# Kernel tuning notes

Hardware: AMD Instinct MI355X
Metric: run time of the kernel (lower is better)

Reference implementation:

```python
import jax, jax.numpy as jnp
import numpy as np

B, N, D = 16, 2048, 1024   # batch, num_windows, input_dim
H, A = 256, 128            # feature head dim, attention hidden dim
EPS = 1e-5                 # torch LayerNorm eps
NEG = -1e9                 # finite mask value (avoids NaN in softmax/grads)
KMAX = max(1, N // 10)     # static upper bound on per-sample top-k


def setup_inputs() -> dict:
    key = jax.random.key(0)
    ks = jax.random.split(key, 6)
    rn = lambda k, shape, sc: jax.random.normal(k, shape, jnp.float32) * sc
    return {
        "x": rn(ks[0], (B, N, D), 1.0),
        "lengths": jax.random.randint(ks[1], (B,), 0, N, dtype=jnp.int64)
                   if jax.config.jax_enable_x64 else
                   jax.random.randint(ks[1], (B,), 0, N, dtype=jnp.int32),
        # feature_head: Linear(D,H) + LayerNorm(H) (+ GELU, dropout=eval no-op)
        "W1": rn(ks[2], (H, D), D ** -0.5), "b1": jnp.zeros((H,), jnp.float32),
        "ln_g": jnp.ones((H,), jnp.float32), "ln_b": jnp.zeros((H,), jnp.float32),
        # attention: Linear(H,A) -> tanh -> Linear(A,1)
        "Wa1": rn(ks[3], (A, H), H ** -0.5), "ba1": jnp.zeros((A,), jnp.float32),
        "Wa2": rn(ks[4], (1, A), A ** -0.5), "ba2": jnp.zeros((1,), jnp.float32),
        # classifier: Linear(H,1)
        "Wc": rn(ks[5], (1, H), H ** -0.5), "bc": jnp.zeros((1,), jnp.float32),
    }


def reference(x, lengths, W1, b1, ln_g, ln_b, Wa1, ba1, Wa2, ba2, Wc, bc):
    # feature head: Linear + LayerNorm + exact GELU (dropout is identity in eval)
    h = jnp.einsum('bnd,hd->bnh', x, W1) + b1
    mu = h.mean(-1, keepdims=True)
    var = h.var(-1, keepdims=True)  # biased, as in torch LayerNorm
    h = (h - mu) * jax.lax.rsqrt(var + EPS) * ln_g + ln_b
    h = jax.nn.gelu(h, approximate=False)

    instance_scores = jnp.einsum('bnh,oh->bno', h, Wc)[..., 0] + bc[0]   # (B, N)
    a_hidden = jnp.tanh(jnp.einsum('bnh,ah->bna', h, Wa1) + ba1)
    attn_logits = jnp.einsum('bna,oa->bno', a_hidden, Wa2)[..., 0] + ba2[0]  # (B, N)

    T = lengths                                    # (B,)
    mask = jnp.arange(N)[None, :] < T[:, None]     # (B, N) valid-window mask

    # masked softmax attention pooling over the first T windows
    w = jax.nn.softmax(jnp.where(mask, attn_logits, NEG), axis=1)
    attn_score = jnp.sum(w * instance_scores * mask, axis=1)

    # dynamic top-k: k = max(1, floor(0.1*T)); take static KMAX then mask ranks
    k_i = jnp.maximum(1, T // 10)                  # (B,)
    vals, _ = jax.lax.top_k(jnp.where(mask, instance_scores, NEG), KMAX)
    rank_mask = jnp.arange(KMAX)[None, :] < k_i[:, None]
    topk_mean = jnp.sum(vals * rank_mask, axis=1) / k_i.astype(vals.dtype)

    video = jnp.where(T > 0, 0.5 * attn_score + 0.5 * topk_mean,
                      jnp.zeros((), vals.dtype))
    return video[:, None], instance_scores
```

## Files before the change

### kernel.cpp

```cpp
#include <hip/hip_runtime.h>
#include <hip/hip_bf16.h>
#include <cmath>

#define Bn 16
#define Nn 2048
#define Dn 1024
#define Hn 256
#define An 128

typedef __bf16 bf16x8 __attribute__((ext_vector_type(8)));
typedef float f32x4 __attribute__((ext_vector_type(4)));
typedef unsigned short ushort8v __attribute__((ext_vector_type(8)));

static __device__ __forceinline__ unsigned short f2bf(float f) {
  unsigned u = __float_as_uint(f);
  u += 0x7fffu + ((u >> 16) & 1u);
  return (unsigned short)(u >> 16);
}

static __device__ __forceinline__ bf16x8 cvt8(const float4 a, const float4 b) {
  bf16x8 r;
  r[0] = (__bf16)a.x; r[1] = (__bf16)a.y; r[2] = (__bf16)a.z; r[3] = (__bf16)a.w;
  r[4] = (__bf16)b.x; r[5] = (__bf16)b.y; r[6] = (__bf16)b.z; r[7] = (__bf16)b.w;
  return r;
}

static __device__ __forceinline__ void glds16(const void* g, void* l) {
  __builtin_amdgcn_global_load_lds(
      (const __attribute__((address_space(1))) unsigned int*)g,
      (__attribute__((address_space(3))) unsigned int*)l, 16, 0, 0);
}

__global__ __launch_bounds__(256) void conv_bf16_kernel(
    const float* __restrict__ W1, const float* __restrict__ Wa1,
    unsigned short* __restrict__ w1o, unsigned short* __restrict__ wa1o) {
  const int bid = blockIdx.x;
  const float* in;
  unsigned short* out;
  int i;
  if (bid < 128) { in = W1;  out = w1o;  i = (bid * 256 + threadIdx.x) << 3; }
  else           { in = Wa1; out = wa1o; i = ((bid - 128) * 256 + threadIdx.x) << 3; }
  const float4 a = *(const float4*)(in + i);
  const float4 b = *(const float4*)(in + i + 4);
  ushort8v u;
  u[0] = f2bf(a.x); u[1] = f2bf(a.y); u[2] = f2bf(a.z); u[3] = f2bf(a.w);
  u[4] = f2bf(b.x); u[5] = f2bf(b.y); u[6] = f2bf(b.z); u[7] = f2bf(b.w);
  *(ushort8v*)(out + i) = u;
}

__global__ __launch_bounds__(256) void fused_main(
    const float* __restrict__ x,
    const float* __restrict__ b1,
    const float* __restrict__ ln_g,
    const float* __restrict__ ln_b,
    const float* __restrict__ ba1,
    const float* __restrict__ Wa2,
    const float* __restrict__ ba2,
    const float* __restrict__ Wc,
    const float* __restrict__ bc,
    const unsigned short* __restrict__ W1bf,
    const unsigned short* __restrict__ Wa1bf,
    float* __restrict__ scores_out,
    float* __restrict__ logits_out)
{
  __shared__ __align__(16) __bf16 AB[4096 + 16384];
  __shared__ float red[64][8];

  const int tid  = threadIdx.x;
  const int wv   = tid >> 6;
  const int lane = tid & 63;
  const int l15  = lane & 15;
  const int lhi  = lane >> 4;
  const int rg   = wv >> 1;
  const int cw   = wv & 1;

  const int gr0 = blockIdx.x << 6;
  const int bb  = blockIdx.x >> 5;
  const int n0  = (blockIdx.x & 31) << 6;

  char* ABb = (char*)AB;

  f32x4 acc[2][8];
  #pragma unroll
  for (int rf = 0; rf < 2; ++rf)
    #pragma unroll
    for (int cf = 0; cf < 8; ++cf)
      acc[rf][cf] = (f32x4){0.f, 0.f, 0.f, 0.f};

  const int st_row   = tid >> 2;
  const int st_lslot = (tid & 3) ^ ((tid >> 3) & 3);
  const float* xbase = x + (size_t)(gr0 + st_row) * Dn + (st_lslot << 3);

  auto issueB = [&](int p, int kc) {
    const int kk = kc << 5;
    char* Bb = ABb + 8192 + p * 16384;
    #pragma unroll
    for (int i = 0; i < 4; ++i) {
      const int c = (wv << 8) + (i << 6) + lane;
      const int h = c >> 2;
      const int lslot = (c & 3) ^ ((c >> 3) & 3);
      glds16(W1bf + (size_t)h * Dn + kk + (lslot << 3),
             ABb + 8192 + p * 16384 + ((wv << 8) + (i << 6)) * 16);
      (void)Bb;
    }
  };

  auto computeStep = [&](int p) {
    const char* Ab = ABb + p * 4096;
    const char* Bb = ABb + 8192 + p * 16384;
    bf16x8 afrag[2];
    #pragma unroll
    for (int rf = 0; rf < 2; ++rf) {
      const int row = (rg << 5) + (rf << 4) + l15;
      afrag[rf] = *(const bf16x8*)(Ab + row * 64 + ((lhi ^ ((row >> 1) & 3)) << 4));
    }
    #pragma unroll
    for (int cf = 0; cf < 8; ++cf) {
      const int h = (cw << 7) + (cf << 4) + l15;
      const bf16x8 bfr = *(const bf16x8*)(Bb + h * 64 + ((lhi ^ ((h >> 1) & 3)) << 4));
      acc[0][cf] = __builtin_amdgcn_mfma_f32_16x16x32_bf16(afrag[0], bfr, acc[0][cf], 0, 0, 0);
      acc[1][cf] = __builtin_amdgcn_mfma_f32_16x16x32_bf16(afrag[1], bfr, acc[1][cf], 0, 0, 0);
    }
  };

  {
    issueB(0, 0);
    const float4 a0 = *(const float4*)(xbase);
    const float4 a1 = *(const float4*)(xbase + 4);
    *(bf16x8*)(ABb + (tid << 4)) = cvt8(a0, a1);
  }
  __syncthreads();

  int p = 0;
  for (int kc = 0; kc < 32; ++kc) {
    const int np = p ^ 1;
    float4 na0, na1;
    if (kc < 31) {
      issueB(np, kc + 1);
      const float* xs = xbase + ((kc + 1) << 5);
      na0 = *(const float4*)(xs);
      na1 = *(const float4*)(xs + 4);
    }
    computeStep(p);
    if (kc < 31)
      *(bf16x8*)(ABb + np * 4096 + (tid << 4)) = cvt8(na0, na1);
    __syncthreads();
    p = np;
  }

  const float bc0 = bc[0];
  float b1v[8];
  #pragma unroll
  for (int cf = 0; cf < 8; ++cf) b1v[cf] = b1[(cw << 7) + (cf << 4) + l15];

  float ps[2][4], ps2[2][4];
  #pragma unroll
  for (int rf = 0; rf < 2; ++rf)
    #pragma unroll
    for (int r = 0; r < 4; ++r) { ps[rf][r] = 0.f; ps2[rf][r] = 0.f; }

  #pragma unroll
  for (int rf = 0; rf < 2; ++rf)
    #pragma unroll
    for (int cf = 0; cf < 8; ++cf)
      #pragma unroll
      for (int r = 0; r < 4; ++r) {
        const float v = acc[rf][cf][r] + b1v[cf];
        acc[rf][cf][r] = v;
        ps[rf][r] += v; ps2[rf][r] += v * v;
      }
  #pragma unroll
  for (int rf = 0; rf < 2; ++rf)
    #pragma unroll
    for (int r = 0; r < 4; ++r)
      #pragma unroll
      for (int s = 1; s < 16; s <<= 1) {
        ps[rf][r]  += __shfl_xor(ps[rf][r],  s, 64);
        ps2[rf][r] += __shfl_xor(ps2[rf][r], s, 64);
      }
  if (l15 == 0) {
    #pragma unroll
    for (int rf = 0; rf < 2; ++rf)
      #pragma unroll
      for (int r = 0; r < 4; ++r) {
        const int rowb = (rg << 5) + (rf << 4) + (lhi << 2) + r;
        red[rowb][cw << 1]       = ps[rf][r];
        red[rowb][(cw << 1) + 1] = ps2[rf][r];
      }
  }
  __syncthreads();

  float mu[2][4], inv[2][4];
  #pragma unroll
  for (int rf = 0; rf < 2; ++rf)
    #pragma unroll
    for (int r = 0; r < 4; ++r) {
      const int rowb = (rg << 5) + (rf << 4) + (lhi << 2) + r;
      const float s = red[rowb][0] + red[rowb][2];
      const float q = red[rowb][1] + red[rowb][3];
      const float m = s * (1.f / 256.f);
      const float var = q * (1.f / 256.f) - m * m;
      mu[rf][r] = m;
      inv[rf][r] = rsqrtf(var + 1e-5f);
    }

  float gv[8], bv[8], wcv[8];
  #pragma unroll
  for (int cf = 0; cf < 8; ++cf) {
    const int col = (cw << 7) + (cf << 4) + l15;
    gv[cf] = ln_g[col]; bv[cf] = ln_b[col]; wcv[cf] = Wc[col];
  }
  float sc[2][4];
  #pragma unroll
  for (int rf = 0; rf < 2; ++rf)
    #pragma unroll
    for (int r = 0; r < 4; ++r) sc[rf][r] = 0.f;

  #pragma unroll
  for (int rf = 0; rf < 2; ++rf)
    #pragma unroll
    for (int cf = 0; cf < 8; ++cf)
      #pragma unroll
      for (int r = 0; r < 4; ++r) {
        float v = (acc[rf][cf][r] - mu[rf][r]) * inv[rf][r] * gv[cf] + bv[cf];
        v = 0.5f * v * (1.f + erff(v * 0.70710678118654752f));
        sc[rf][r] += v * wcv[cf];
        const int rowb = (rg << 5) + (rf << 4) + (lhi << 2) + r;
        const int col  = (cw << 7) + (cf << 4) + l15;
        *(__bf16*)(ABb + rowb * 512 + (((col >> 3) ^ (rowb & 7)) << 4) + ((col & 7) << 1)) = (__bf16)v;
      }
  #pragma unroll
  for (int rf = 0; rf < 2; ++rf)
    #pragma unroll
    for (int r = 0; r < 4; ++r)
      #pragma unroll
      for (int s = 1; s < 16; s <<= 1)
        sc[rf][r] += __shfl_xor(sc[rf][r], s, 64);
  if (l15 == 0) {
    #pragma unroll
    for (int rf = 0; rf < 2; ++rf)
      #pragma unroll
      for (int r = 0; r < 4; ++r) {
        const int rowb = (rg << 5) + (rf << 4) + (lhi << 2) + r;
        red[rowb][4 + cw] = sc[rf][r];
      }
  }
  __syncthreads();
  if (tid < 64)
    scores_out[(size_t)bb * Nn + n0 + tid] = red[tid][4] + red[tid][5] + bc0;

  f32x4 acc2[8];
  #pragma unroll
  for (int cf = 0; cf < 8; ++cf) acc2[cf] = (f32x4){0.f, 0.f, 0.f, 0.f};

  const int r16 = (wv << 4) + l15;
  #pragma unroll
  for (int ks = 0; ks < 8; ++ks) {
    const bf16x8 af = *(const bf16x8*)(ABb + r16 * 512 + ((((ks << 2) + lhi) ^ (r16 & 7)) << 4));
    #pragma unroll
    for (int cf = 0; cf < 8; ++cf) {
      const bf16x8 bfr = *(const bf16x8*)((const __bf16*)Wa1bf +
                          (size_t)((cf << 4) + l15) * Hn + (ks << 5) + (lhi << 3));
      acc2[cf] = __builtin_amdgcn_mfma_f32_16x16x32_bf16(af, bfr, acc2[cf], 0, 0, 0);
    }
  }
  const float ba20 = ba2[0];
  float lg[4] = {0.f, 0.f, 0.f, 0.f};
  #pragma unroll
  for (int cf = 0; cf < 8; ++cf) {
    const int col = (cf << 4) + l15;
    const float bav = ba1[col], w2v = Wa2[col];
    #pragma unroll
    for (int r = 0; r < 4; ++r) {
      const float t = acc2[cf][r] + bav;
      const float e = __expf(2.f * t);
      const float th = 1.f - 2.f / (e + 1.f);
      lg[r] += th * w2v;
    }
  }
  #pragma unroll
  for (int r = 0; r < 4; ++r)
    #pragma unroll
    for (int s = 1; s < 16; s <<= 1) lg[r] += __shfl_xor(lg[r], s, 64);
  if (l15 == 0) {
    #pragma unroll
    for (int r = 0; r < 4; ++r)
      logits_out[(size_t)bb * Nn + n0 + (wv << 4) + (lhi << 2) + r] = lg[r] + ba20;
  }
}

__global__ __launch_bounds__(256) void finalize_kernel(
    const int* __restrict__ lengths,
    const float* __restrict__ scores,
    const float* __restrict__ logits,
    float* __restrict__ video)
{
  const int b = blockIdx.x;
  const int tid = threadIdx.x;
  __shared__ float sS[Nn];
  __shared__ float sL[Nn];
  __shared__ unsigned skey[Nn];
  __shared__ float sred[8];

  const int T = lengths[b];
  for (int i = tid; i < Nn; i += 256) {
    sS[i] = scores[(size_t)b * Nn + i];
    sL[i] = logits[(size_t)b * Nn + i];
  }
  __syncthreads();
  if (T <= 0) { if (tid == 0) video[b] = 0.f; return; }

  float m = -3.0e38f;
  for (int i = tid; i < T; i += 256) m = fmaxf(m, sL[i]);
  #pragma unroll
  for (int s = 1; s < 64; s <<= 1) m = fmaxf(m, __shfl_xor(m, s, 64));
  if ((tid & 63) == 0) sred[tid >> 6] = m;
  __syncthreads();
  m = fmaxf(fmaxf(sred[0], sred[1]), fmaxf(sred[2], sred[3]));
  __syncthreads();

  float se = 0.f, swe = 0.f;
  for (int i = tid; i < T; i += 256) {
    const float e = expf(sL[i] - m);
    se += e; swe += e * sS[i];
  }
  #pragma unroll
  for (int s = 1; s < 64; s <<= 1) { se += __shfl_xor(se, s, 64); swe += __shfl_xor(swe, s, 64); }
  if ((tid & 63) == 0) { sred[tid >> 6] = se; sred[4 + (tid >> 6)] = swe; }
  __syncthreads();
  se  = sred[0] + sred[1] + sred[2] + sred[3];
  swe = sred[4] + sred[5] + sred[6] + sred[7];
  __syncthreads();
  const float attn = swe / se;

  for (int i = tid; i < T; i += 256) {
    const unsigned u = __float_as_uint(sS[i]);
    skey[i] = (u & 0x80000000u) ? ~u : (u | 0x80000000u);
  }
  __syncthreads();
  const int k = max(1, T / 10);
  unsigned ans = 0u;
  for (int bit = 31; bit >= 0; --bit) {
    const unsigned cand = ans | (1u << bit);
    int c = 0;
    for (int i = tid; i < T; i += 256) c += (skey[i] >= cand) ? 1 : 0;
    #pragma unroll
    for (int s = 1; s < 64; s <<= 1) c += __shfl_xor(c, s, 64);
    if ((tid & 63) == 0) sred[tid >> 6] = (float)c;
    __syncthreads();
    c = (int)(sred[0] + sred[1] + sred[2] + sred[3]);
    __syncthreads();
    if (c >= k) ans = cand;
  }
  int cgt = 0; float sgt = 0.f;
  for (int i = tid; i < T; i += 256) {
    if (skey[i] > ans) { cgt++; sgt += sS[i]; }
  }
  #pragma unroll
  for (int s = 1; s < 64; s <<= 1) { cgt += __shfl_xor(cgt, s, 64); sgt += __shfl_xor(sgt, s, 64); }
  if ((tid & 63) == 0) { sred[tid >> 6] = (float)cgt; sred[4 + (tid >> 6)] = sgt; }
  __syncthreads();
  cgt = (int)(sred[0] + sred[1] + sred[2] + sred[3]);
  sgt = sred[4] + sred[5] + sred[6] + sred[7];

  const unsigned ub = (ans & 0x80000000u) ? (ans ^ 0x80000000u) : ~ans;
  const float kth = __uint_as_float(ub);
  const float topk = (sgt + (float)(k - cgt) * kth) / (float)k;
  if (tid == 0) video[b] = 0.5f * attn + 0.5f * topk;
}

extern "C" void kernel_launch(void* const* d_in, const int* in_sizes, int n_in,
                              void* d_out, int out_size, void* d_ws, size_t ws_size,
                              hipStream_t stream) {
  const float* x    = (const float*)d_in[0];
  const int*   len  = (const int*)  d_in[1];
  const float* W1   = (const float*)d_in[2];
  const float* b1   = (const float*)d_in[3];
  const float* ln_g = (const float*)d_in[4];
  const float* ln_b = (const float*)d_in[5];
  const float* Wa1  = (const float*)d_in[6];
  const float* ba1  = (const float*)d_in[7];
  const float* Wa2  = (const float*)d_in[8];
  const float* ba2  = (const float*)d_in[9];
  const float* Wc   = (const float*)d_in[10];
  const float* bc   = (const float*)d_in[11];

  float* out    = (float*)d_out;
  float* video  = out;
  float* scores = out + Bn;

  char* ws = (char*)d_ws;
  float*          logits = (float*)ws;
  unsigned short* wa1bf  = (unsigned short*)(ws + (size_t)Bn * Nn * 4);
  unsigned short* w1bf   = (unsigned short*)(ws + (size_t)Bn * Nn * 4 + (size_t)An * Hn * 2);

  hipLaunchKernelGGL(conv_bf16_kernel, dim3(144), dim3(256), 0, stream, W1, Wa1, w1bf, wa1bf);
  hipLaunchKernelGGL(fused_main, dim3(Bn * Nn / 64), dim3(256), 0, stream,
                     x, b1, ln_g, ln_b, ba1, Wa2, ba2, Wc, bc,
                     w1bf, wa1bf, scores, logits);
  hipLaunchKernelGGL(finalize_kernel, dim3(Bn), dim3(256), 0, stream, len, scores, logits, video);
}
```

Baseline: 95.69 us.

## Double K-tile to 64, prefetch x two stages ahead with explicit waitcnt barriers

The GEMM main loop now uses a 64-wide K chunk (16 iterations instead of 32), with a new 8-way XOR swizzle for the A and B LDS tiles. x rows are register-prefetched two chunks ahead and the barriers are replaced by explicit s_waitcnt vmcnt/lgkmcnt plus s_barrier, with sched_barriers to pin the issue order. The aim is to halve barrier count and hide global-load latency better. In exchange LDS use grows to 80KB, which limits occupancy, and register pressure rises from the extra prefetch buffers.

```diff
diff --git a/kernel.cpp b/kernel.cpp
--- a/kernel.cpp
+++ b/kernel.cpp
@@ -11,6 +11,17 @@
 typedef __bf16 bf16x8 __attribute__((ext_vector_type(8)));
 typedef float f32x4 __attribute__((ext_vector_type(4)));
 typedef unsigned short ushort8v __attribute__((ext_vector_type(8)));
+
+#define LDSA(p) ((p) * 8192)
+#define LDSB(p) (16384 + (p) * 32768)
+#define LDSH    49152
+#define LDSRED  8192
+
+#define PIPE_BARRIER(N) do {                                        \
+    asm volatile("s_waitcnt vmcnt(" #N ") lgkmcnt(0)" ::: "memory"); \
+    __builtin_amdgcn_s_barrier();                                   \
+    __builtin_amdgcn_sched_barrier(0);                              \
+  } while (0)
 
 static __device__ __forceinline__ unsigned short f2bf(float f) {
   unsigned u = __float_as_uint(f);
@@ -63,8 +74,7 @@
     float* __restrict__ scores_out,
     float* __restrict__ logits_out)
 {
-  __shared__ __align__(16) __bf16 AB[4096 + 16384];
-  __shared__ float red[64][8];
+  __shared__ __align__(16) char lds[81920];
 
   const int tid  = threadIdx.x;
   const int wv   = tid >> 6;
@@ -78,8 +88,6 @@
   const int bb  = blockIdx.x >> 5;
   const int n0  = (blockIdx.x & 31) << 6;
 
-  char* ABb = (char*)AB;
-
   f32x4 acc[2][8];
   #pragma unroll
   for (int rf = 0; rf < 2; ++rf)
@@ -87,66 +95,76 @@
     for (int cf = 0; cf < 8; ++cf)
       acc[rf][cf] = (f32x4){0.f, 0.f, 0.f, 0.f};
 
-  const int st_row   = tid >> 2;
-  const int st_lslot = (tid & 3) ^ ((tid >> 3) & 3);
-  const float* xbase = x + (size_t)(gr0 + st_row) * Dn + (st_lslot << 3);
+  const int arow = tid >> 2;
+  const int aq   = tid & 3;
+  const float* xbase = x + (size_t)(gr0 + arow) * Dn + (aq << 4);
+  char* awr0 = lds + arow * 128 + (((aq << 1)       ^ (arow & 7)) << 4);
+  char* awr1 = lds + arow * 128 + ((((aq << 1) | 1) ^ (arow & 7)) << 4);
+
+  const unsigned short* bsrc = W1bf + (size_t)(wv * 64 + (lane >> 3)) * Dn
+                               + (((lane & 7) ^ ((lane >> 3) & 7)) << 3);
+
+  const int axor = l15 & 7;
 
   auto issueB = [&](int p, int kc) {
-    const int kk = kc << 5;
-    char* Bb = ABb + 8192 + p * 16384;
-    #pragma unroll
-    for (int i = 0; i < 4; ++i) {
-      const int c = (wv << 8) + (i << 6) + lane;
-      const int h = c >> 2;
-      const int lslot = (c & 3) ^ ((c >> 3) & 3);
-      glds16(W1bf + (size_t)h * Dn + kk + (lslot << 3),
-             ABb + 8192 + p * 16384 + ((wv << 8) + (i << 6)) * 16);
-      (void)Bb;
+    #pragma unroll
+    for (int i = 0; i < 8; ++i)
+      glds16(bsrc + (size_t)i * 8 * Dn + (kc << 6),
+             lds + LDSB(p) + (wv * 64 + i * 8) * 128);
+  };
+  auto loadX = [&](float4* v, int kc) {
+    #pragma unroll
+    for (int j = 0; j < 4; ++j)
+      v[j] = *(const float4*)(xbase + (kc << 6) + (j << 2));
+  };
+  auto writeA = [&](int p, const float4* v) {
+    *(bf16x8*)(awr0 + LDSA(p)) = cvt8(v[0], v[1]);
+    *(bf16x8*)(awr1 + LDSA(p)) = cvt8(v[2], v[3]);
+  };
+  auto computeStep = [&](int p) {
+    const char* Ab = lds + LDSA(p);
+    const char* Bb = lds + LDSB(p);
+    #pragma unroll
+    for (int ks = 0; ks < 2; ++ks) {
+      const int so = (((ks << 2) + lhi) ^ axor) << 4;
+      const bf16x8 aA = *(const bf16x8*)(Ab + ((rg << 5) + l15) * 128 + so);
+      const bf16x8 aB = *(const bf16x8*)(Ab + ((rg << 5) + 16 + l15) * 128 + so);
+      #pragma unroll
+      for (int cf = 0; cf < 8; ++cf) {
+        const bf16x8 bfr = *(const bf16x8*)(Bb + ((cw << 7) + (cf << 4) + l15) * 128 + so);
+        acc[0][cf] = __builtin_amdgcn_mfma_f32_16x16x32_bf16(aA, bfr, acc[0][cf], 0, 0, 0);
+        acc[1][cf] = __builtin_amdgcn_mfma_f32_16x16x32_bf16(aB, bfr, acc[1][cf], 0, 0, 0);
+      }
     }
   };
 
-  auto computeStep = [&](int p) {
-    const char* Ab = ABb + p * 4096;
-    const char* Bb = ABb + 8192 + p * 16384;
-    bf16x8 afrag[2];
-    #pragma unroll
-    for (int rf = 0; rf < 2; ++rf) {
-      const int row = (rg << 5) + (rf << 4) + l15;
-      afrag[rf] = *(const bf16x8*)(Ab + row * 64 + ((lhi ^ ((row >> 1) & 3)) << 4));
+  float4 xr0[4], xr1[4];
+  issueB(0, 0);
+  __builtin_amdgcn_sched_barrier(0);
+  loadX(xr0, 0);
+  loadX(xr1, 1);
+  __builtin_amdgcn_sched_barrier(0);
+  writeA(0, xr0);
+  PIPE_BARRIER(4);
+
+  #pragma unroll
+  for (int kc = 0; kc < 16; ++kc) {
+    const int p = kc & 1;
+    const int np = p ^ 1;
+    if (kc < 15) issueB(np, kc + 1);
+    __builtin_amdgcn_sched_barrier(0);
+    if (kc < 14) loadX((kc & 1) ? xr1 : xr0, kc + 2);
+    __builtin_amdgcn_sched_barrier(0);
+    computeStep(p);
+    if (kc < 15) {
+      writeA(np, np ? xr1 : xr0);
+      if (kc < 14) PIPE_BARRIER(4);
+      else         PIPE_BARRIER(0);
     }
-    #pragma unroll
-    for (int cf = 0; cf < 8; ++cf) {
-      const int h = (cw << 7) + (cf << 4) + l15;
-      const bf16x8 bfr = *(const bf16x8*)(Bb + h * 64 + ((lhi ^ ((h >> 1) & 3)) << 4));
-      acc[0][cf] = __builtin_amdgcn_mfma_f32_16x16x32_bf16(afrag[0], bfr, acc[0][cf], 0, 0, 0);
-      acc[1][cf] = __builtin_amdgcn_mfma_f32_16x16x32_bf16(afrag[1], bfr, acc[1][cf], 0, 0, 0);
-    }
-  };
-
-  {
-    issueB(0, 0);
-    const float4 a0 = *(const float4*)(xbase);
-    const float4 a1 = *(const float4*)(xbase + 4);
-    *(bf16x8*)(ABb + (tid << 4)) = cvt8(a0, a1);
-  }
-  __syncthreads();
-
-  int p = 0;
-  for (int kc = 0; kc < 32; ++kc) {
-    const int np = p ^ 1;
-    float4 na0, na1;
-    if (kc < 31) {
-      issueB(np, kc + 1);
-      const float* xs = xbase + ((kc + 1) << 5);
-      na0 = *(const float4*)(xs);
-      na1 = *(const float4*)(xs + 4);
-    }
-    computeStep(p);
-    if (kc < 31)
-      *(bf16x8*)(ABb + np * 4096 + (tid << 4)) = cvt8(na0, na1);
-    __syncthreads();
-    p = np;
-  }
+  }
+  __syncthreads();
+
+  float (*red)[8] = (float(*)[8])(lds + LDSRED);
 
   const float bc0 = bc[0];
   float b1v[8];
@@ -227,7 +245,8 @@
         sc[rf][r] += v * wcv[cf];
         const int rowb = (rg << 5) + (rf << 4) + (lhi << 2) + r;
         const int col  = (cw << 7) + (cf << 4) + l15;
-        *(__bf16*)(ABb + rowb * 512 + (((col >> 3) ^ (rowb & 7)) << 4) + ((col & 7) << 1)) = (__bf16)v;
+        *(__bf16*)(lds + LDSH + rowb * 512 + (((col >> 3) ^ (rowb & 7)) << 4)
+                   + ((col & 7) << 1)) = (__bf16)v;
       }
   #pragma unroll
   for (int rf = 0; rf < 2; ++rf)
@@ -256,7 +275,8 @@
   const int r16 = (wv << 4) + l15;
   #pragma unroll
   for (int ks = 0; ks < 8; ++ks) {
-    const bf16x8 af = *(const bf16x8*)(ABb + r16 * 512 + ((((ks << 2) + lhi) ^ (r16 & 7)) << 4));
+    const bf16x8 af = *(const bf16x8*)(lds + LDSH + r16 * 512 +
+                        ((((ks << 2) + lhi) ^ (r16 & 7)) << 4));
     #pragma unroll
     for (int cf = 0; cf < 8; ++cf) {
       const bf16x8 bfr = *(const bf16x8*)((const __bf16*)Wa1bf +
```

Result: faster. 88.90 us (-7.1%).

## Restructure GEMM mainloop: register-direct W1 loads, 256-wide x chunks in LDS

Applied to the files above, without the earlier changes.

Rewrites the main GEMM pipeline. W1 bf16 fragments are now loaded straight from global memory into registers, double-buffered one k-step ahead, instead of being staged through LDS with global_load_lds. x is loaded in 256-column chunks into 16 float4 registers and written to a double-buffered 64 KB LDS region, so a barrier is needed only every 8 k-steps rather than every step. The aim is fewer barriers and less LDS traffic, at the cost of higher register pressure and LDS use, which may lower occupancy, plus redundant global W1 loads per wave.

```diff
diff --git a/kernel.cpp b/kernel.cpp
--- a/kernel.cpp
+++ b/kernel.cpp
@@ -12,6 +12,12 @@
 typedef float f32x4 __attribute__((ext_vector_type(4)));
 typedef unsigned short ushort8v __attribute__((ext_vector_type(8)));
 
+#define LDS_BARRIER do {                                   \
+    asm volatile("s_waitcnt lgkmcnt(0)" ::: "memory");     \
+    __builtin_amdgcn_s_barrier();                          \
+    __builtin_amdgcn_sched_barrier(0);                     \
+  } while (0)
+
 static __device__ __forceinline__ unsigned short f2bf(float f) {
   unsigned u = __float_as_uint(f);
   u += 0x7fffu + ((u >> 16) & 1u);
@@ -23,12 +29,6 @@
   r[0] = (__bf16)a.x; r[1] = (__bf16)a.y; r[2] = (__bf16)a.z; r[3] = (__bf16)a.w;
   r[4] = (__bf16)b.x; r[5] = (__bf16)b.y; r[6] = (__bf16)b.z; r[7] = (__bf16)b.w;
   return r;
-}
-
-static __device__ __forceinline__ void glds16(const void* g, void* l) {
-  __builtin_amdgcn_global_load_lds(
-      (const __attribute__((address_space(1))) unsigned int*)g,
-      (__attribute__((address_space(3))) unsigned int*)l, 16, 0, 0);
 }
 
 __global__ __launch_bounds__(256) void conv_bf16_kernel(
@@ -63,8 +63,7 @@
     float* __restrict__ scores_out,
     float* __restrict__ logits_out)
 {
-  __shared__ __align__(16) __bf16 AB[4096 + 16384];
-  __shared__ float red[64][8];
+  __shared__ __align__(16) char lds[65536 + 2048];
 
   const int tid  = threadIdx.x;
   const int wv   = tid >> 6;
@@ -78,8 +77,6 @@
   const int bb  = blockIdx.x >> 5;
   const int n0  = (blockIdx.x & 31) << 6;
 
-  char* ABb = (char*)AB;
-
   f32x4 acc[2][8];
   #pragma unroll
   for (int rf = 0; rf < 2; ++rf)
@@ -87,66 +84,64 @@
     for (int cf = 0; cf < 8; ++cf)
       acc[rf][cf] = (f32x4){0.f, 0.f, 0.f, 0.f};
 
-  const int st_row   = tid >> 2;
-  const int st_lslot = (tid & 3) ^ ((tid >> 3) & 3);
-  const float* xbase = x + (size_t)(gr0 + st_row) * Dn + (st_lslot << 3);
-
-  auto issueB = [&](int p, int kc) {
-    const int kk = kc << 5;
-    char* Bb = ABb + 8192 + p * 16384;
-    #pragma unroll
-    for (int i = 0; i < 4; ++i) {
-      const int c = (wv << 8) + (i << 6) + lane;
-      const int h = c >> 2;
-      const int lslot = (c & 3) ^ ((c >> 3) & 3);
-      glds16(W1bf + (size_t)h * Dn + kk + (lslot << 3),
-             ABb + 8192 + p * 16384 + ((wv << 8) + (i << 6)) * 16);
-      (void)Bb;
+  const int sr = tid >> 2, sq = tid & 3;
+  const float* xbase = x + (size_t)(gr0 + sr) * Dn + (sq << 6);
+  char* awbase = lds + sr * 512;
+
+  const int arow0 = (rg << 5) + l15;
+  const int arow1 = arow0 + 16;
+  const int ax    = l15 & 7;
+
+  const __bf16* wbL = (const __bf16*)W1bf + (size_t)((cw << 7) + l15) * Dn + (lhi << 3);
+
+  float4 xr[16];
+  bf16x8 Ba[8], Bb[8];
+
+  #define LOADX(ph) do {                                                     \
+      _Pragma("unroll") for (int j = 0; j < 16; ++j)                         \
+        xr[j] = *(const float4*)(xbase + ((ph) << 8) + (j << 2));            \
+    } while (0)
+  #define WRITEA(pbuf) do {                                                  \
+      char* ab_ = awbase + (pbuf) * 32768;                                   \
+      _Pragma("unroll") for (int j = 0; j < 8; ++j) {                        \
+        const bf16x8 v_ = cvt8(xr[2 * j], xr[2 * j + 1]);                    \
+        *(bf16x8*)(ab_ + ((((sq << 3) + j) ^ (sr & 7)) << 4)) = v_;          \
+      }                                                                      \
+    } while (0)
+  #define ISSUEB(arr, Kk) do {                                               \
+      const __bf16* bp_ = wbL + ((Kk) << 5);                                 \
+      _Pragma("unroll") for (int cf = 0; cf < 8; ++cf)                       \
+        arr[cf] = *(const bf16x8*)(bp_ + (size_t)(cf << 4) * Dn);            \
+    } while (0)
+  #define DOMFMA(arr, Kk) do {                                               \
+      const char* ab_ = lds + (((Kk) >> 3) & 1) * 32768;                     \
+      const int sl_ = ((Kk) & 7) << 2;                                       \
+      const bf16x8 a0_ = *(const bf16x8*)(ab_ + arow0 * 512 + (((sl_ + lhi) ^ ax) << 4)); \
+      const bf16x8 a1_ = *(const bf16x8*)(ab_ + arow1 * 512 + (((sl_ + lhi) ^ ax) << 4)); \
+      _Pragma("unroll") for (int cf = 0; cf < 8; ++cf) {                     \
+        acc[0][cf] = __builtin_amdgcn_mfma_f32_16x16x32_bf16(a0_, arr[cf], acc[0][cf], 0, 0, 0); \
+        acc[1][cf] = __builtin_amdgcn_mfma_f32_16x16x32_bf16(a1_, arr[cf], acc[1][cf], 0, 0, 0); \
+      }                                                                      \
+    } while (0)
+
+  LOADX(0);
+  ISSUEB(Ba, 0);
+  WRITEA(0);
+  LDS_BARRIER;
+
+  #pragma unroll
+  for (int K = 0; K < 32; ++K) {
+    if (K < 31) { if (K & 1) ISSUEB(Ba, K + 1); else ISSUEB(Bb, K + 1); }
+    if ((K & 7) == 0 && K < 24) LOADX((K >> 3) + 1);
+    if (K & 1) DOMFMA(Bb, K); else DOMFMA(Ba, K);
+    if ((K & 7) == 7 && K < 31) {
+      WRITEA(((K >> 3) + 1) & 1);
+      LDS_BARRIER;
     }
-  };
-
-  auto computeStep = [&](int p) {
-    const char* Ab = ABb + p * 4096;
-    const char* Bb = ABb + 8192 + p * 16384;
-    bf16x8 afrag[2];
-    #pragma unroll
-    for (int rf = 0; rf < 2; ++rf) {
-      const int row = (rg << 5) + (rf << 4) + l15;
-      afrag[rf] = *(const bf16x8*)(Ab + row * 64 + ((lhi ^ ((row >> 1) & 3)) << 4));
-    }
-    #pragma unroll
-    for (int cf = 0; cf < 8; ++cf) {
-      const int h = (cw << 7) + (cf << 4) + l15;
-      const bf16x8 bfr = *(const bf16x8*)(Bb + h * 64 + ((lhi ^ ((h >> 1) & 3)) << 4));
-      acc[0][cf] = __builtin_amdgcn_mfma_f32_16x16x32_bf16(afrag[0], bfr, acc[0][cf], 0, 0, 0);
-      acc[1][cf] = __builtin_amdgcn_mfma_f32_16x16x32_bf16(afrag[1], bfr, acc[1][cf], 0, 0, 0);
-    }
-  };
-
-  {
-    issueB(0, 0);
-    const float4 a0 = *(const float4*)(xbase);
-    const float4 a1 = *(const float4*)(xbase + 4);
-    *(bf16x8*)(ABb + (tid << 4)) = cvt8(a0, a1);
-  }
-  __syncthreads();
-
-  int p = 0;
-  for (int kc = 0; kc < 32; ++kc) {
-    const int np = p ^ 1;
-    float4 na0, na1;
-    if (kc < 31) {
-      issueB(np, kc + 1);
-      const float* xs = xbase + ((kc + 1) << 5);
-      na0 = *(const float4*)(xs);
-      na1 = *(const float4*)(xs + 4);
-    }
-    computeStep(p);
-    if (kc < 31)
-      *(bf16x8*)(ABb + np * 4096 + (tid << 4)) = cvt8(na0, na1);
-    __syncthreads();
-    p = np;
-  }
+  }
+  __syncthreads();
+
+  float (*red)[8] = (float(*)[8])(lds + 65536);
 
   const float bc0 = bc[0];
   float b1v[8];
@@ -227,7 +222,8 @@
         sc[rf][r] += v * wcv[cf];
         const int rowb = (rg << 5) + (rf << 4) + (lhi << 2) + r;
         const int col  = (cw << 7) + (cf << 4) + l15;
-        *(__bf16*)(ABb + rowb * 512 + (((col >> 3) ^ (rowb & 7)) << 4) + ((col & 7) << 1)) = (__bf16)v;
+        *(__bf16*)(lds + rowb * 512 + (((col >> 3) ^ (rowb & 7)) << 4)
+                   + ((col & 7) << 1)) = (__bf16)v;
       }
   #pragma unroll
   for (int rf = 0; rf < 2; ++rf)
@@ -256,7 +252,8 @@
   const int r16 = (wv << 4) + l15;
   #pragma unroll
   for (int ks = 0; ks < 8; ++ks) {
-    const bf16x8 af = *(const bf16x8*)(ABb + r16 * 512 + ((((ks << 2) + lhi) ^ (r16 & 7)) << 4));
+    const bf16x8 af = *(const bf16x8*)(lds + r16 * 512 +
+                        ((((ks << 2) + lhi) ^ (r16 & 7)) << 4));
     #pragma unroll
     for (int cf = 0; cf < 8; ++cf) {
       const bf16x8 bfr = *(const bf16x8*)((const __bf16*)Wa1bf +
```

Result: slower. 137.5 us (+43.7%).

## Split attention GEMM into separate kernel and prepack swizzled weights for register-staged loads

Applied to the files above, without the earlier changes.

Weights are prepacked on device into the exact swizzled LDS tile order, so the main GEMM loads B with plain coalesced vector loads staged through registers instead of global_load_lds. The loop is fully unrolled with s_setprio, uses a lighter lgkmcnt barrier, and raises occupancy to three blocks per CU. The attention-hidden GEMM moves into a second kernel that reads a bf16 h buffer from global memory and keeps Wa1 in LDS. This trades an extra 16 MB write and read of h and one more launch for a lighter main kernel.

```diff
diff --git a/kernel.cpp b/kernel.cpp
--- a/kernel.cpp
+++ b/kernel.cpp
@@ -11,6 +11,13 @@
 typedef __bf16 bf16x8 __attribute__((ext_vector_type(8)));
 typedef float f32x4 __attribute__((ext_vector_type(4)));
 typedef unsigned short ushort8v __attribute__((ext_vector_type(8)));
+typedef unsigned int uint4v __attribute__((ext_vector_type(4)));
+
+#define LDS_BARRIER do {                                   \
+    asm volatile("s_waitcnt lgkmcnt(0)" ::: "memory");     \
+    __builtin_amdgcn_s_barrier();                          \
+    __builtin_amdgcn_sched_barrier(0);                     \
+  } while (0)
 
 static __device__ __forceinline__ unsigned short f2bf(float f) {
   unsigned u = __float_as_uint(f);
@@ -25,46 +32,50 @@
   return r;
 }
 
-static __device__ __forceinline__ void glds16(const void* g, void* l) {
-  __builtin_amdgcn_global_load_lds(
-      (const __attribute__((address_space(1))) unsigned int*)g,
-      (__attribute__((address_space(3))) unsigned int*)l, 16, 0, 0);
-}
-
-__global__ __launch_bounds__(256) void conv_bf16_kernel(
+__global__ __launch_bounds__(256) void pack_weights(
     const float* __restrict__ W1, const float* __restrict__ Wa1,
-    unsigned short* __restrict__ w1o, unsigned short* __restrict__ wa1o) {
-  const int bid = blockIdx.x;
-  const float* in;
-  unsigned short* out;
-  int i;
-  if (bid < 128) { in = W1;  out = w1o;  i = (bid * 256 + threadIdx.x) << 3; }
-  else           { in = Wa1; out = wa1o; i = ((bid - 128) * 256 + threadIdx.x) << 3; }
-  const float4 a = *(const float4*)(in + i);
-  const float4 b = *(const float4*)(in + i + 4);
-  ushort8v u;
-  u[0] = f2bf(a.x); u[1] = f2bf(a.y); u[2] = f2bf(a.z); u[3] = f2bf(a.w);
-  u[4] = f2bf(b.x); u[5] = f2bf(b.y); u[6] = f2bf(b.z); u[7] = f2bf(b.w);
-  *(ushort8v*)(out + i) = u;
-}
-
-__global__ __launch_bounds__(256) void fused_main(
+    unsigned short* __restrict__ w1p, unsigned short* __restrict__ wa1p) {
+  const int idx = blockIdx.x * 256 + threadIdx.x;
+  const float* src;
+  unsigned short* dst;
+  if (blockIdx.x < 128) {
+    const int kc  = idx >> 10;
+    const int u   = idx & 1023;
+    const int col = u >> 2;
+    const int lq  = (u & 3) ^ ((col >> 1) & 3);
+    src = W1 + (size_t)col * Dn + (kc << 5) + (lq << 3);
+    dst = w1p + (size_t)idx * 8;
+  } else {
+    const int v   = idx - 32768;
+    const int row = v >> 5;
+    const int ls  = (v & 31) ^ (row & 7);
+    src = Wa1 + (size_t)row * Hn + (ls << 3);
+    dst = wa1p + (size_t)v * 8;
+  }
+  const float4 a = *(const float4*)src;
+  const float4 b = *(const float4*)(src + 4);
+  ushort8v o;
+  o[0] = f2bf(a.x); o[1] = f2bf(a.y); o[2] = f2bf(a.z); o[3] = f2bf(a.w);
+  o[4] = f2bf(b.x); o[5] = f2bf(b.y); o[6] = f2bf(b.z); o[7] = f2bf(b.w);
+  *(ushort8v*)dst = o;
+}
+
+#define K1A(p) ((p) * 4096)
+#define K1B(p) (8192 + (p) * 16384)
+#define K1H    8192
+#define K1RED  40960
+__global__ __launch_bounds__(256, 3) void gemm_ln_kernel(
     const float* __restrict__ x,
     const float* __restrict__ b1,
     const float* __restrict__ ln_g,
     const float* __restrict__ ln_b,
-    const float* __restrict__ ba1,
-    const float* __restrict__ Wa2,
-    const float* __restrict__ ba2,
     const float* __restrict__ Wc,
     const float* __restrict__ bc,
-    const unsigned short* __restrict__ W1bf,
-    const unsigned short* __restrict__ Wa1bf,
+    const unsigned short* __restrict__ w1p,
     float* __restrict__ scores_out,
-    float* __restrict__ logits_out)
+    unsigned short* __restrict__ h_out)
 {
-  __shared__ __align__(16) __bf16 AB[4096 + 16384];
-  __shared__ float red[64][8];
+  __shared__ __align__(16) char lds[43008];
 
   const int tid  = threadIdx.x;
   const int wv   = tid >> 6;
@@ -75,10 +86,8 @@
   const int cw   = wv & 1;
 
   const int gr0 = blockIdx.x << 6;
-  const int bb  = blockIdx.x >> 5;
-  const int n0  = (blockIdx.x & 31) << 6;
-
-  char* ABb = (char*)AB;
+  const int bb  = gr0 >> 11;
+  const int n0  = gr0 & (Nn - 1);
 
   f32x4 acc[2][8];
   #pragma unroll
@@ -87,66 +96,66 @@
     for (int cf = 0; cf < 8; ++cf)
       acc[rf][cf] = (f32x4){0.f, 0.f, 0.f, 0.f};
 
-  const int st_row   = tid >> 2;
-  const int st_lslot = (tid & 3) ^ ((tid >> 3) & 3);
-  const float* xbase = x + (size_t)(gr0 + st_row) * Dn + (st_lslot << 3);
-
-  auto issueB = [&](int p, int kc) {
-    const int kk = kc << 5;
-    char* Bb = ABb + 8192 + p * 16384;
-    #pragma unroll
-    for (int i = 0; i < 4; ++i) {
-      const int c = (wv << 8) + (i << 6) + lane;
-      const int h = c >> 2;
-      const int lslot = (c & 3) ^ ((c >> 3) & 3);
-      glds16(W1bf + (size_t)h * Dn + kk + (lslot << 3),
-             ABb + 8192 + p * 16384 + ((wv << 8) + (i << 6)) * 16);
-      (void)Bb;
+  const int arow = tid >> 2, aq = tid & 3;
+  const int aphys = aq ^ ((arow >> 1) & 3);
+  const float* xsrc = x + (size_t)(gr0 + arow) * Dn + (aq << 3);
+  const int awoff = arow * 64 + (aphys << 4);
+
+  const unsigned short* bsrc = w1p + (size_t)tid * 8;
+
+  const int bx    = lhi ^ ((l15 >> 1) & 3);
+  const int aoff  = ((rg << 5) + l15) * 64 + (bx << 4);
+  const int boff  = (((cw << 7) + l15) * 64) + (bx << 4);
+
+  float4 xs0, xs1;
+  uint4v Bst[4];
+
+  auto loadStage = [&](int kc) {
+    xs0 = *(const float4*)(xsrc + (kc << 5));
+    xs1 = *(const float4*)(xsrc + (kc << 5) + 4);
+    const unsigned short* bp = bsrc + (size_t)kc * 8192;
+    #pragma unroll
+    for (int q = 0; q < 4; ++q)
+      Bst[q] = *(const uint4v*)(bp + q * 2048);
+  };
+  auto writeStage = [&](int p) {
+    *(bf16x8*)(lds + K1A(p) + awoff) = cvt8(xs0, xs1);
+    #pragma unroll
+    for (int q = 0; q < 4; ++q)
+      *(uint4v*)(lds + K1B(p) + ((q << 8) + tid) * 16) = Bst[q];
+  };
+  auto computeStep = [&](int p) {
+    const char* Ab = lds + K1A(p);
+    const char* Bb = lds + K1B(p);
+    __builtin_amdgcn_s_setprio(1);
+    const bf16x8 aA = *(const bf16x8*)(Ab + aoff);
+    const bf16x8 aB = *(const bf16x8*)(Ab + aoff + 1024);
+    #pragma unroll
+    for (int cf = 0; cf < 8; ++cf) {
+      const bf16x8 bfr = *(const bf16x8*)(Bb + boff + cf * 1024);
+      acc[0][cf] = __builtin_amdgcn_mfma_f32_16x16x32_bf16(aA, bfr, acc[0][cf], 0, 0, 0);
+      acc[1][cf] = __builtin_amdgcn_mfma_f32_16x16x32_bf16(aB, bfr, acc[1][cf], 0, 0, 0);
     }
+    __builtin_amdgcn_s_setprio(0);
   };
 
-  auto computeStep = [&](int p) {
-    const char* Ab = ABb + p * 4096;
-    const char* Bb = ABb + 8192 + p * 16384;
-    bf16x8 afrag[2];
-    #pragma unroll
-    for (int rf = 0; rf < 2; ++rf) {
-      const int row = (rg << 5) + (rf << 4) + l15;
-      afrag[rf] = *(const bf16x8*)(Ab + row * 64 + ((lhi ^ ((row >> 1) & 3)) << 4));
+  loadStage(0);
+  writeStage(0);
+  LDS_BARRIER;
+
+  #pragma unroll
+  for (int kc = 0; kc < 32; ++kc) {
+    const int p = kc & 1;
+    if (kc < 31) loadStage(kc + 1);
+    computeStep(p);
+    if (kc < 31) {
+      writeStage(p ^ 1);
+      LDS_BARRIER;
     }
-    #pragma unroll
-    for (int cf = 0; cf < 8; ++cf) {
-      const int h = (cw << 7) + (cf << 4) + l15;
-      const bf16x8 bfr = *(const bf16x8*)(Bb + h * 64 + ((lhi ^ ((h >> 1) & 3)) << 4));
-      acc[0][cf] = __builtin_amdgcn_mfma_f32_16x16x32_bf16(afrag[0], bfr, acc[0][cf], 0, 0, 0);
-      acc[1][cf] = __builtin_amdgcn_mfma_f32_16x16x32_bf16(afrag[1], bfr, acc[1][cf], 0, 0, 0);
-    }
-  };
-
-  {
-    issueB(0, 0);
-    const float4 a0 = *(const float4*)(xbase);
-    const float4 a1 = *(const float4*)(xbase + 4);
-    *(bf16x8*)(ABb + (tid << 4)) = cvt8(a0, a1);
-  }
-  __syncthreads();
-
-  int p = 0;
-  for (int kc = 0; kc < 32; ++kc) {
-    const int np = p ^ 1;
-    float4 na0, na1;
-    if (kc < 31) {
-      issueB(np, kc + 1);
-      const float* xs = xbase + ((kc + 1) << 5);
-      na0 = *(const float4*)(xs);
-      na1 = *(const float4*)(xs + 4);
-    }
-    computeStep(p);
-    if (kc < 31)
-      *(bf16x8*)(ABb + np * 4096 + (tid << 4)) = cvt8(na0, na1);
-    __syncthreads();
-    p = np;
-  }
+  }
+  __syncthreads();
+
+  float (*red)[8] = (float(*)[8])(lds + K1RED);
 
   const float bc0 = bc[0];
   float b1v[8];
@@ -227,7 +236,8 @@
         sc[rf][r] += v * wcv[cf];
         const int rowb = (rg << 5) + (rf << 4) + (lhi << 2) + r;
         const int col  = (cw << 7) + (cf << 4) + l15;
-        *(__bf16*)(ABb + rowb * 512 + (((col >> 3) ^ (rowb & 7)) << 4) + ((col & 7) << 1)) = (__bf16)v;
+        *(__bf16*)(lds + K1H + rowb * 512 + (((col >> 3) ^ (rowb & 7)) << 4)
+                   + ((col & 7) << 1)) = (__bf16)v;
       }
   #pragma unroll
   for (int rf = 0; rf < 2; ++rf)
@@ -249,18 +259,61 @@
   if (tid < 64)
     scores_out[(size_t)bb * Nn + n0 + tid] = red[tid][4] + red[tid][5] + bc0;
 
+  #pragma unroll
+  for (int j = 0; j < 8; ++j) {
+    const int g   = (j << 8) + tid;
+    const int row = g >> 5;
+    const int c   = g & 31;
+    const bf16x8 hv = *(const bf16x8*)(lds + K1H + row * 512 +
+                                       ((c ^ (row & 7)) << 4));
+    *(bf16x8*)(h_out + (size_t)(gr0 + row) * 256 + (c << 3)) = hv;
+  }
+}
+
+__global__ __launch_bounds__(512) void stage2_kernel(
+    const unsigned short* __restrict__ h_in,
+    const unsigned short* __restrict__ wa1p,
+    const float* __restrict__ ba1,
+    const float* __restrict__ Wa2,
+    const float* __restrict__ ba2,
+    float* __restrict__ logits_out)
+{
+  __shared__ __align__(16) char lds2[65536];
+
+  const int tid  = threadIdx.x;
+  const int wv   = tid >> 6;
+  const int lane = tid & 63;
+  const int l15  = lane & 15;
+  const int lhi  = lane >> 4;
+
+  const int gr0 = blockIdx.x << 7;
+  const int bb  = gr0 >> 11;
+  const int n0  = gr0 & (Nn - 1);
+
+  {
+    uint4v st[8];
+    #pragma unroll
+    for (int j = 0; j < 8; ++j)
+      st[j] = *(const uint4v*)(wa1p + (size_t)((j << 9) + tid) * 8);
+    #pragma unroll
+    for (int j = 0; j < 8; ++j)
+      *(uint4v*)(lds2 + ((j << 9) + tid) * 16) = st[j];
+  }
+  __syncthreads();
+
   f32x4 acc2[8];
   #pragma unroll
   for (int cf = 0; cf < 8; ++cf) acc2[cf] = (f32x4){0.f, 0.f, 0.f, 0.f};
 
-  const int r16 = (wv << 4) + l15;
+  const unsigned short* hrow = h_in + (size_t)(gr0 + (wv << 4) + l15) * 256 + (lhi << 3);
   #pragma unroll
   for (int ks = 0; ks < 8; ++ks) {
-    const bf16x8 af = *(const bf16x8*)(ABb + r16 * 512 + ((((ks << 2) + lhi) ^ (r16 & 7)) << 4));
+    const bf16x8 af = *(const bf16x8*)(hrow + (ks << 5));
     #pragma unroll
     for (int cf = 0; cf < 8; ++cf) {
-      const bf16x8 bfr = *(const bf16x8*)((const __bf16*)Wa1bf +
-                          (size_t)((cf << 4) + l15) * Hn + (ks << 5) + (lhi << 3));
+      const int row2 = (cf << 4) + l15;
+      const bf16x8 bfr = *(const bf16x8*)(lds2 + row2 * 512 +
+                          ((((ks << 2) + lhi) ^ (row2 & 7)) << 4));
       acc2[cf] = __builtin_amdgcn_mfma_f32_16x16x32_bf16(af, bfr, acc2[cf], 0, 0, 0);
     }
   }
@@ -391,12 +444,14 @@
 
   char* ws = (char*)d_ws;
   float*          logits = (float*)ws;
-  unsigned short* wa1bf  = (unsigned short*)(ws + (size_t)Bn * Nn * 4);
-  unsigned short* w1bf   = (unsigned short*)(ws + (size_t)Bn * Nn * 4 + (size_t)An * Hn * 2);
-
-  hipLaunchKernelGGL(conv_bf16_kernel, dim3(144), dim3(256), 0, stream, W1, Wa1, w1bf, wa1bf);
-  hipLaunchKernelGGL(fused_main, dim3(Bn * Nn / 64), dim3(256), 0, stream,
-                     x, b1, ln_g, ln_b, ba1, Wa2, ba2, Wc, bc,
-                     w1bf, wa1bf, scores, logits);
+  unsigned short* h_g    = (unsigned short*)(ws + 131072);
+  unsigned short* w1p    = (unsigned short*)(ws + 131072 + 16777216);
+  unsigned short* wa1p   = (unsigned short*)(ws + 131072 + 16777216 + 524288);
+
+  hipLaunchKernelGGL(pack_weights, dim3(144), dim3(256), 0, stream, W1, Wa1, w1p, wa1p);
+  hipLaunchKernelGGL(gemm_ln_kernel, dim3(Bn * Nn / 64), dim3(256), 0, stream,
+                     x, b1, ln_g, ln_b, Wc, bc, w1p, scores, h_g);
+  hipLaunchKernelGGL(stage2_kernel, dim3(Bn * Nn / 128), dim3(512), 0, stream,
+                     h_g, wa1p, ba1, Wa2, ba2, logits);
   hipLaunchKernelGGL(finalize_kernel, dim3(Bn), dim3(256), 0, stream, len, scores, logits, video);
 }
```

After: 87.40 us. -8.7%, faster.
